# Performance work log

Hardware: AMD Instinct MI355X
Metric: run time of the kernel (lower is better)

## Reference

```python
import jax, jax.numpy as jnp
import numpy as np

B, T, E, H = 2, 2048, 1024, 16
D = E // H            # head dim = 64
ROT = D // 2          # rotary_dim = 32 (only first half of head dim is rotated)
THETA = 10000.0


def _rope(x):
    # x: (B, H, T, D). Faithful to rotary_embedding_torch.rotate_queries_or_keys
    # with dim=ROT: rotate first ROT features, interleaved-pair style, pass rest.
    t = x.shape[-2]
    inv = 1.0 / (THETA ** (jnp.arange(0, ROT, 2, dtype=jnp.float32) / ROT))   # (ROT//2,)
    freqs = jnp.arange(t, dtype=jnp.float32)[:, None] * inv[None, :]          # (T, ROT//2)
    freqs = jnp.repeat(freqs, 2, axis=-1)                                      # (T, ROT)
    cos, sin = jnp.cos(freqs), jnp.sin(freqs)
    xr, xp = x[..., :ROT], x[..., ROT:]
    p = xr.reshape(*xr.shape[:-1], ROT // 2, 2)
    rot = jnp.stack((-p[..., 1], p[..., 0]), axis=-1).reshape(xr.shape)
    return jnp.concatenate([xr * cos + rot * sin, xp], axis=-1)


def setup_inputs() -> dict:
    key = jax.random.key(0)
    k1, k2, k3 = jax.random.split(key, 3)
    query = jax.random.normal(k1, (B, T, E), dtype=jnp.float32)
    inputs = {
        "query": query,
        "key": query,            # ignored (cross_attention=False)
        "value": query,          # ignored
        "padding_mask": jnp.ones((B, T), dtype=bool),
        "in_proj_weight": jax.random.uniform(k2, (3 * E, E), dtype=jnp.float32),
        "out_proj_weight": jax.random.normal(k3, (E, E), dtype=jnp.float32) * (E ** -0.5),
    }
    return inputs


def reference(query, key, value, padding_mask, in_proj_weight, out_proj_weight):
    # cross_attention=False: key/value are overwritten by query
    key = query
    value = query
    q = query @ in_proj_weight[:E].T
    k = key @ in_proj_weight[E:2 * E].T
    v = value @ in_proj_weight[2 * E:].T
    # NOTE: raw reshape (B,T,E)->(B,H,T,D), exactly as in the torch module
    q = q.reshape(B, H, T, D)
    k = k.reshape(B, H, T, D)
    v = v.reshape(B, H, T, D)
    q = _rope(q)
    k = _rope(k)   # causal self-attention path: rotate keys too
    causal = jnp.tril(jnp.ones((T, T), dtype=bool))                 # (T, T)
    mask = causal[None, None] & padding_mask[:, None, None, :]      # (B,1,T,T) -> broadcast over H
    scores = jnp.einsum("bhqd,bhkd->bhqk", q, k) / jnp.sqrt(jnp.float32(D))
    scores = jnp.where(mask, scores, -jnp.inf)
    attn = jax.nn.softmax(scores, axis=-1)
    x = jnp.einsum("bhqk,bhkd->bhqd", attn, v)
    x = x.reshape(B, T, E)      # raw reshape back, as in torch
    return x @ out_proj_weight.T
```

## Files before the change

### kernel.cpp

```cpp
#include <hip/hip_runtime.h>
#include <stdint.h>

#define T_ 2048
#define E_ 1024

typedef __attribute__((ext_vector_type(8))) __bf16 bf16x8;
typedef __attribute__((ext_vector_type(4))) float f32x4;

__device__ __forceinline__ void gload_lds16(const void* g, void* l) {
  __builtin_amdgcn_global_load_lds(
      (const __attribute__((address_space(1))) unsigned int*)g,
      (__attribute__((address_space(3))) unsigned int*)l, 16, 0, 0);
}

__global__ __launch_bounds__(256) void k_prep(const float4* __restrict__ q,
                                              ushort4* __restrict__ xh,
                                              ushort4* __restrict__ xl,
                                              const float4* __restrict__ win,
                                              ushort4* __restrict__ whh,
                                              ushort4* __restrict__ whl,
                                              const float4* __restrict__ wout,
                                              ushort4* __restrict__ wob,
                                              float2* __restrict__ cs) {
  const int b = blockIdx.x, tid = threadIdx.x;
  if (b < 7168) {
    const float4* src;
    ushort4 *hi, *lo;
    int i;
    if (b < 4096) { src = q; hi = xh; lo = xl; i = b * 256 + tid; }
    else          { src = win; hi = whh; lo = whl; i = (b - 4096) * 256 + tid; }
    float4 x = src[i];
    float xs[4] = {x.x, x.y, x.z, x.w};
    union { __bf16 bb[4]; ushort4 u; } H, L;
#pragma unroll
    for (int jj = 0; jj < 4; ++jj) {
      __bf16 h = (__bf16)xs[jj];
      H.bb[jj] = h;
      L.bb[jj] = (__bf16)(xs[jj] - (float)h);
    }
    hi[i] = H.u;
    lo[i] = L.u;
  } else if (b < 8192) {
    int i = (b - 7168) * 256 + tid;
    float4 x = wout[i];
    float xs[4] = {x.x, x.y, x.z, x.w};
    union { __bf16 bb[4]; ushort4 u; } H;
#pragma unroll
    for (int jj = 0; jj < 4; ++jj) H.bb[jj] = (__bf16)xs[jj];
    wob[i] = H.u;
  } else {
    int i = (b - 8192) * 256 + tid;
    int t = i >> 4, f = i & 15;
    double inv = pow(10000.0, -(double)f / 16.0);
    double ang = (double)t * inv;
    cs[i] = make_float2((float)cos(ang), (float)sin(ang));
  }
}

__global__ __launch_bounds__(256) void k_proj(const __bf16* __restrict__ xh,
                                              const __bf16* __restrict__ xl,
                                              const __bf16* __restrict__ whh,
                                              const __bf16* __restrict__ whl,
                                              const float2* __restrict__ cs,
                                              __bf16* __restrict__ qhi,
                                              __bf16* __restrict__ qlo,
                                              __bf16* __restrict__ khi,
                                              __bf16* __restrict__ klo,
                                              __bf16* __restrict__ v16t) {
  __shared__ __align__(16) __bf16 AsH[128 * 64];
  __shared__ __align__(16) __bf16 BsH[128 * 64];
  __shared__ __align__(16) __bf16 AsL[128 * 64];
  __shared__ __align__(16) __bf16 BsL[128 * 64];
  const int tid = threadIdx.x, lane = tid & 63, w = tid >> 6;
  const int g = lane >> 4, d = lane & 15;
  const int lr8 = lane >> 3;
  const int swz8 = ((lane & 7) ^ lr8) * 8;
  const int rsl = d & 7;
  const int K = 1024;

  if (blockIdx.x < 512) {
    const int bi = blockIdx.x;
    const int bx = (bi >> 3) & 15;
    const int by = ((bi & 7) << 2) | ((bi >> 7) & 3);
    const int wm = w >> 1, wn = w & 1;
    const int m0 = by * 128, n0 = bx * 128;

    f32x4 acc[4][4];
#pragma unroll
    for (int i = 0; i < 4; ++i)
#pragma unroll
      for (int j = 0; j < 4; ++j) acc[i][j] = (f32x4)(0.0f);

    for (int k0 = 0; k0 < K; k0 += 64) {
      __syncthreads();
#pragma unroll
      for (int c = 0; c < 4; ++c) {
        const int rr = c * 32 + w * 8 + lr8;
        const int ldo = (c * 32 + w * 8) * 64;
        gload_lds16(xh + (size_t)(m0 + rr) * K + k0 + swz8, &AsH[ldo]);
        gload_lds16(xl + (size_t)(m0 + rr) * K + k0 + swz8, &AsL[ldo]);
        gload_lds16(whh + (size_t)(n0 + rr) * K + k0 + swz8, &BsH[ldo]);
        gload_lds16(whl + (size_t)(n0 + rr) * K + k0 + swz8, &BsL[ldo]);
      }
      __syncthreads();
#pragma unroll
      for (int k2 = 0; k2 < 2; ++k2) {
        const int sl = ((k2 * 4 + g) ^ rsl) * 8;
        bf16x8 bh[4], bl[4];
#pragma unroll
        for (int j = 0; j < 4; ++j) {
          const int r = wn * 64 + j * 16 + d;
          bh[j] = *(const bf16x8*)&BsH[r * 64 + sl];
          bl[j] = *(const bf16x8*)&BsL[r * 64 + sl];
        }
#pragma unroll
        for (int i = 0; i < 4; ++i) {
          const int r = wm * 64 + i * 16 + d;
          const bf16x8 ahf = *(const bf16x8*)&AsH[r * 64 + sl];
          const bf16x8 alf = *(const bf16x8*)&AsL[r * 64 + sl];
#pragma unroll
          for (int j = 0; j < 4; ++j) {
            acc[i][j] = __builtin_amdgcn_mfma_f32_16x16x32_bf16(ahf, bh[j], acc[i][j], 0, 0, 0);
            acc[i][j] = __builtin_amdgcn_mfma_f32_16x16x32_bf16(alf, bh[j], acc[i][j], 0, 0, 0);
            acc[i][j] = __builtin_amdgcn_mfma_f32_16x16x32_bf16(ahf, bl[j], acc[i][j], 0, 0, 0);
          }
        }
      }
    }

#pragma unroll
    for (int i = 0; i < 4; ++i) {
      const int rbase = m0 + (w >> 1) * 64 + i * 16 + g * 4;
#pragma unroll
      for (int j = 0; j < 4; ++j) {
        const int col = n0 + (w & 1) * 64 + j * 16 + d;
#pragma unroll
        for (int r = 0; r < 4; ++r) {
          const float vv = acc[i][j][r];
          const int row = rbase + r;
          const float xp = __shfl_xor(vv, 1);
          const int which = col >> 10;
          const int cl = col & 1023;
          const int d2 = cl & 63;
          const int t2 = (row & 127) * 16 + (cl >> 6);
          float y;
          if (d2 < 32) {
            const float2 cse = cs[t2 * 16 + (d2 >> 1)];
            y = (d2 & 1) ? (vv * cse.x + xp * cse.y) : (vv * cse.x - xp * cse.y);
          } else {
            y = vv;
          }
          if (which == 0) y *= 0.18033688011112042f;
          const __bf16 hi = (__bf16)y;
          const __bf16 lo = (__bf16)(y - (float)hi);
          const size_t off = (size_t)row * 1024 + cl;
          (which ? khi : qhi)[off] = hi;
          (which ? klo : qlo)[off] = lo;
        }
      }
    }
  } else {
    const int bi = blockIdx.x - 512;
    const int bx = (bi >> 3) & 7;
    const int by = ((bi & 7) << 3) | ((bi >> 6) & 7);
    const int m0 = by * 64, n0 = bx * 128;
    const __bf16* Bv = whh + (size_t)2048 * 1024;

    f32x4 acc[4][2];
#pragma unroll
    for (int i = 0; i < 4; ++i)
#pragma unroll
      for (int j = 0; j < 2; ++j) acc[i][j] = (f32x4)(0.0f);

    for (int k0 = 0; k0 < K; k0 += 64) {
      __syncthreads();
#pragma unroll
      for (int c = 0; c < 2; ++c) {
        const int rr = c * 32 + w * 8 + lr8;
        gload_lds16(xh + (size_t)(m0 + rr) * K + k0 + swz8, &AsH[(c * 32 + w * 8) * 64]);
      }
#pragma unroll
      for (int c = 0; c < 4; ++c) {
        const int rr = c * 32 + w * 8 + lr8;
        gload_lds16(Bv + (size_t)(n0 + rr) * K + k0 + swz8, &BsH[(c * 32 + w * 8) * 64]);
      }
      __syncthreads();
#pragma unroll
      for (int k2 = 0; k2 < 2; ++k2) {
        const int sl = ((k2 * 4 + g) ^ rsl) * 8;
        bf16x8 bh[2], ah[4];
#pragma unroll
        for (int j = 0; j < 2; ++j)
          bh[j] = *(const bf16x8*)&BsH[(w * 32 + j * 16 + d) * 64 + sl];
#pragma unroll
        for (int i = 0; i < 4; ++i)
          ah[i] = *(const bf16x8*)&AsH[(i * 16 + d) * 64 + sl];
#pragma unroll
        for (int i = 0; i < 4; ++i)
#pragma unroll
          for (int j = 0; j < 2; ++j)
            acc[i][j] = __builtin_amdgcn_mfma_f32_16x16x32_bf16(ah[i], bh[j], acc[i][j], 0, 0, 0);
      }
    }

#pragma unroll
    for (int i = 0; i < 4; ++i) {
      const int rbase = m0 + i * 16 + g * 4;
#pragma unroll
      for (int j = 0; j < 2; ++j) {
        const int col = n0 + w * 32 + j * 16 + d;
#pragma unroll
        for (int r = 0; r < 4; ++r) {
          const int row = rbase + r;
          const int p = row >> 7;
          const int tp = ((row & 127) << 4) | (col >> 6);
          const int dp = col & 63;
          v16t[((size_t)p * 64 + dp) * 2048 + tp] = (__bf16)acc[i][j][r];
        }
      }
    }
  }
}

__global__ __launch_bounds__(256) void k_gemmout(const __bf16* __restrict__ Ah,
                                                 const __bf16* __restrict__ Bh,
                                                 float* __restrict__ C32) {
  __shared__ __align__(16) __bf16 As[64 * 64];
  __shared__ __align__(16) __bf16 Bs[128 * 64];
  const int bi = blockIdx.x;
  const int bx = (bi >> 3) & 7;
  const int by = ((bi & 7) << 3) | ((bi >> 6) & 7);
  const int tid = threadIdx.x, lane = tid & 63, w = tid >> 6;
  const int g = lane >> 4, d = lane & 15;
  const int m0 = by * 64, n0 = bx * 128;
  const int K = 1024, N = 1024;

  f32x4 acc[4][2];
#pragma unroll
  for (int i = 0; i < 4; ++i)
#pragma unroll
    for (int j = 0; j < 2; ++j) acc[i][j] = (f32x4)(0.0f);

  const int lr8 = lane >> 3;
  const int swz8 = ((lane & 7) ^ lr8) * 8;
  const int rsl = d & 7;

  for (int k0 = 0; k0 < K; k0 += 64) {
    __syncthreads();
#pragma unroll
    for (int c = 0; c < 2; ++c) {
      const int rr = c * 32 + w * 8 + lr8;
      gload_lds16(Ah + (size_t)(m0 + rr) * K + k0 + swz8, &As[(c * 32 + w * 8) * 64]);
    }
#pragma unroll
    for (int c = 0; c < 4; ++c) {
      const int rr = c * 32 + w * 8 + lr8;
      gload_lds16(Bh + (size_t)(n0 + rr) * K + k0 + swz8, &Bs[(c * 32 + w * 8) * 64]);
    }
    __syncthreads();
#pragma unroll
    for (int k2 = 0; k2 < 2; ++k2) {
      const int sl = ((k2 * 4 + g) ^ rsl) * 8;
      bf16x8 bh[2], ah[4];
#pragma unroll
      for (int j = 0; j < 2; ++j)
        bh[j] = *(const bf16x8*)&Bs[(w * 32 + j * 16 + d) * 64 + sl];
#pragma unroll
      for (int i = 0; i < 4; ++i)
        ah[i] = *(const bf16x8*)&As[(i * 16 + d) * 64 + sl];
#pragma unroll
      for (int i = 0; i < 4; ++i)
#pragma unroll
        for (int j = 0; j < 2; ++j)
          acc[i][j] = __builtin_amdgcn_mfma_f32_16x16x32_bf16(ah[i], bh[j], acc[i][j], 0, 0, 0);
    }
  }

#pragma unroll
  for (int i = 0; i < 4; ++i) {
    const int rbase = m0 + i * 16 + g * 4;
#pragma unroll
    for (int j = 0; j < 2; ++j) {
      const int col = n0 + w * 32 + j * 16 + d;
#pragma unroll
      for (int r = 0; r < 4; ++r)
        C32[(size_t)(rbase + r) * N + col] = acc[i][j][r];
    }
  }
}

__global__ __launch_bounds__(512, 4) void k_attn(const __bf16* __restrict__ qhi,
                                                 const __bf16* __restrict__ qlo,
                                                 const __bf16* __restrict__ khi,
                                                 const __bf16* __restrict__ klo,
                                                 const __bf16* __restrict__ v16t,
                                                 __bf16* __restrict__ x16,
                                                 float* __restrict__ po,
                                                 float* __restrict__ pm,
                                                 float* __restrict__ pl_) {
  __shared__ __align__(16) __bf16 KH[2][64 * 64];
  __shared__ __align__(16) __bf16 KL[2][64 * 64];
  __shared__ __align__(16) __bf16 VT[2][64 * 64];
  __shared__ __align__(16) __bf16 PL[8][16 * 72];

  const int bi = blockIdx.x;
  const int b = (bi >> 3) & 15;
  const int panel = (bi & 7) | (((bi >> 7) & 3) << 3);
  const int u0 = 9 * b;
  int qtA = 0;
  while (2 * (qtA + 1) * (qtA + 2) <= u0) ++qtA;
  const int cumA = 2 * qtA * (qtA + 1);
  const int cumB = 2 * (qtA + 1) * (qtA + 2);
  const int jloA = u0 - cumA;
  const bool two = (u0 + 9 > cumB);
  const int jhiA = two ? (cumB - 1 - cumA) : (u0 + 8 - cumA);
  const int jhiB = u0 + 8 - cumB;

  const int tid = threadIdx.x, lane = tid & 63, w = tid >> 6;
  const int g = lane >> 4, d = lane & 15;
  const size_t hb = (size_t)panel * T_ * 64;

  const int kr = tid >> 3, kc = tid & 7;
  const int swz = (kc ^ (kr & 7)) * 8;
  const __bf16* kB = khi + hb;
  const __bf16* lB = klo + hb;
  const __bf16* vB = v16t + (size_t)panel * (64 * T_);

#define STAGE(j, bb)                                                        \
  {                                                                         \
    gload_lds16(kB + (size_t)((j) * 64 + kr) * 64 + swz, &KH[bb][w * 512]); \
    gload_lds16(lB + (size_t)((j) * 64 + kr) * 64 + swz, &KL[bb][w * 512]); \
    gload_lds16(vB + (size_t)kr * T_ + (j) * 64 + swz, &VT[bb][w * 512]);   \
  }

  int cur = 0;
  STAGE(jloA, 0);

  for (int seg = 0; seg < 2; ++seg) {
    if (seg && !two) break;
    const int qt = qtA + seg;
    const int jlo = seg ? 0 : jloA;
    const int jhi = seg ? jhiB : jhiA;
    const int q0 = qt << 8;

    bf16x8 qh[2][2], ql[2][2];
#pragma unroll
    for (int rb = 0; rb < 2; ++rb) {
      const int rbi = w * 2 + rb;
      const size_t qrow = hb + (size_t)(q0 + rbi * 16 + d) * 64;
      qh[rb][0] = *(const bf16x8*)&qhi[qrow + g * 8];
      qh[rb][1] = *(const bf16x8*)&qhi[qrow + 32 + g * 8];
      ql[rb][0] = *(const bf16x8*)&qlo[qrow + g * 8];
      ql[rb][1] = *(const bf16x8*)&qlo[qrow + 32 + g * 8];
    }

    f32x4 o[2][4];
#pragma unroll
    for (int rb = 0; rb < 2; ++rb)
#pragma unroll
      for (int i = 0; i < 4; ++i) o[rb][i] = (f32x4)(0.0f);
    float m_[2] = {-__builtin_inff(), -__builtin_inff()};
    float l_[2] = {0.0f, 0.0f};

    for (int j = jlo; j <= jhi; ++j) {
      __syncthreads();
      if (j < jhi) {
        STAGE(j + 1, cur ^ 1);
      } else if (!seg && two) {
        STAGE(0, cur ^ 1);
      }

#pragma unroll
      for (int rb = 0; rb < 2; ++rb) {
        const int rbi = w * 2 + rb;
        const int qrow0 = q0 + rbi * 16;
        if (j * 64 > qrow0 + 15) continue;

        f32x4 s[4];
        __builtin_amdgcn_s_setprio(1);
#pragma unroll
        for (int f = 0; f < 4; ++f) {
          f32x4 accs = (f32x4)(0.0f);
          const int colr = f * 16 + d;
#pragma unroll
          for (int ds = 0; ds < 2; ++ds) {
            const int slot = ((ds * 4 + g) ^ (colr & 7)) * 8;
            const bf16x8 kf = *(const bf16x8*)&KH[cur][colr * 64 + slot];
            const bf16x8 lf = *(const bf16x8*)&KL[cur][colr * 64 + slot];
            accs = __builtin_amdgcn_mfma_f32_16x16x32_bf16(kf, qh[rb][ds], accs, 0, 0, 0);
            accs = __builtin_amdgcn_mfma_f32_16x16x32_bf16(kf, ql[rb][ds], accs, 0, 0, 0);
            accs = __builtin_amdgcn_mfma_f32_16x16x32_bf16(lf, qh[rb][ds], accs, 0, 0, 0);
          }
          s[f] = accs;
        }
        __builtin_amdgcn_s_setprio(0);

        if (j * 64 + 63 > qrow0) {
          const int qq = qrow0 + d;
#pragma unroll
          for (int f = 0; f < 4; ++f)
#pragma unroll
            for (int r = 0; r < 4; ++r) {
              const int kv = j * 64 + f * 16 + g * 4 + r;
              if (kv > qq) s[f][r] = -30000.0f;
            }
        }

        float pmax = fmaxf(fmaxf(s[0][0], s[0][1]), fmaxf(s[0][2], s[0][3]));
#pragma unroll
        for (int f = 1; f < 4; ++f)
          pmax = fmaxf(pmax, fmaxf(fmaxf(s[f][0], s[f][1]), fmaxf(s[f][2], s[f][3])));
        pmax = fmaxf(pmax, __shfl_xor(pmax, 16));
        pmax = fmaxf(pmax, __shfl_xor(pmax, 32));

        if (!__all(pmax - m_[rb] <= 11.5f)) {
          const float mnew = fmaxf(m_[rb], pmax);
          const float fac = exp2f(m_[rb] - mnew);
          m_[rb] = mnew;
          float facr[4];
#pragma unroll
          for (int r = 0; r < 4; ++r)
            facr[r] = __shfl(fac, (lane & 48) | (g * 4 + r));
#pragma unroll
          for (int ni = 0; ni < 4; ++ni)
#pragma unroll
            for (int r = 0; r < 4; ++r) o[rb][ni][r] *= facr[r];
          l_[rb] *= fac;
        }

        float sum = 0.0f;
#pragma unroll
        for (int f = 0; f < 4; ++f) {
          union { __bf16 bb[4]; ushort4 u4; } pk;
#pragma unroll
          for (int r = 0; r < 4; ++r) {
            const float pv = exp2f(s[f][r] - m_[rb]);
            sum += pv;
            pk.bb[r] = (__bf16)pv;
          }
          *(ushort4*)&PL[w][d * 72 + f * 16 + g * 4] = pk.u4;
        }
        sum += __shfl_xor(sum, 16);
        sum += __shfl_xor(sum, 32);
        l_[rb] += sum;

        __builtin_amdgcn_s_setprio(1);
#pragma unroll
        for (int ks = 0; ks < 2; ++ks) {
          const bf16x8 pa = *(const bf16x8*)&PL[w][d * 72 + ks * 32 + g * 8];
#pragma unroll
          for (int ni = 0; ni < 4; ++ni) {
            const bf16x8 vf =
                *(const bf16x8*)&VT[cur][(ni * 16 + d) * 64 + (((ks * 4 + g) ^ (d & 7)) * 8)];
            o[rb][ni] = __builtin_amdgcn_mfma_f32_16x16x32_bf16(pa, vf, o[rb][ni], 0, 0, 0);
          }
        }
        __builtin_amdgcn_s_setprio(0);
      }
      cur ^= 1;
    }

    if (jlo == 0 && jhi == 4 * qt + 3) {
#pragma unroll
      for (int rb = 0; rb < 2; ++rb) {
        const int rbi = w * 2 + rb;
        float lr[4];
#pragma unroll
        for (int r = 0; r < 4; ++r)
          lr[r] = __shfl(l_[rb], (lane & 48) | (g * 4 + r));
#pragma unroll
        for (int ni = 0; ni < 4; ++ni)
#pragma unroll
          for (int r = 0; r < 4; ++r) {
            const size_t row = hb + (size_t)(q0 + rbi * 16 + g * 4 + r) * 64;
            x16[row + ni * 16 + d] = (__bf16)(o[rb][ni][r] / lr[r]);
          }
      }
    } else {
      const int slot = panel * 23 + b + qt;
#pragma unroll
      for (int rb = 0; rb < 2; ++rb) {
        const int rbi = w * 2 + rb;
#pragma unroll
        for (int ni = 0; ni < 4; ++ni)
#pragma unroll
          for (int r = 0; r < 4; ++r) {
            const int rowin = rbi * 16 + g * 4 + r;
            po[(size_t)slot * 16384 + rowin * 64 + ni * 16 + d] = o[rb][ni][r];
          }
        if (g == 0) {
          pm[slot * 256 + rbi * 16 + d] = m_[rb];
          pl_[slot * 256 + rbi * 16 + d] = l_[rb];
        }
      }
    }
  }
#undef STAGE
}

__global__ __launch_bounds__(256) void k_combine(const float* __restrict__ po,
                                                 const float* __restrict__ pm,
                                                 const float* __restrict__ pl_,
                                                 __bf16* __restrict__ x16) {
  const int bi = blockIdx.x;
  const int p = (bi & 7) | ((bi / 3584) << 3);
  const int li = ((bi >> 3) % 448) * 256 + threadIdx.x;
  const int d = li & 63;
  const int t2 = 256 + (li >> 6);
  const int qt = t2 >> 8;
  const int rowin = t2 & 255;
  const int cq = 2 * qt * (qt + 1);
  const int nc = (cq + 4 * qt + 3) / 9 - cq / 9 + 1;
  const int s0 = p * 23 + cq / 9 + qt;
  float M = -__builtin_inff();
  for (int s = 0; s < nc; ++s) M = fmaxf(M, pm[(s0 + s) * 256 + rowin]);
  float L = 0.0f, O = 0.0f;
  for (int s = 0; s < nc; ++s) {
    const float ww = exp2f(pm[(s0 + s) * 256 + rowin] - M);
    L += pl_[(s0 + s) * 256 + rowin] * ww;
    O += po[(size_t)(s0 + s) * 16384 + rowin * 64 + d] * ww;
  }
  x16[((size_t)p * T_ + t2) * 64 + d] = (__bf16)(O / L);
}

extern "C" void kernel_launch(void* const* d_in, const int* in_sizes, int n_in,
                              void* d_out, int out_size, void* d_ws, size_t ws_size,
                              hipStream_t stream) {
  const float* query = (const float*)d_in[0];
  const float* win = (const float*)d_in[4];
  const float* wout = (const float*)d_in[5];
  float* out = (float*)d_out;

  const size_t MB = 1024 * 1024;
  const size_t KB = 1024;
  char* ws = (char*)d_ws;
  __bf16* xh = (__bf16*)(ws);
  __bf16* xl = (__bf16*)(ws + 8 * MB);
  __bf16* whh = (__bf16*)(ws + 16 * MB);
  __bf16* whl = (__bf16*)(ws + 22 * MB);
  float* po = (float*)(ws);
  __bf16* v16t = (__bf16*)(ws + 46 * MB);
  __bf16* qhi = (__bf16*)(ws + 54 * MB);
  __bf16* qlo = (__bf16*)(ws + 62 * MB);
  __bf16* khi = (__bf16*)(ws + 70 * MB);
  __bf16* klo = (__bf16*)(ws + 78 * MB);
  __bf16* wob = (__bf16*)(ws + 86 * MB);
  float* pm = (float*)(ws + 88 * MB);
  float* pl_ = (float*)(ws + 88 * MB + 768 * KB);
  float2* cs = (float2*)(ws + 89 * MB + 512 * KB);
  __bf16* x16 = (__bf16*)(ws + 54 * MB);

  k_prep<<<8320, 256, 0, stream>>>((const float4*)query, (ushort4*)xh, (ushort4*)xl,
                                   (const float4*)win, (ushort4*)whh, (ushort4*)whl,
                                   (const float4*)wout, (ushort4*)wob, cs);

  k_proj<<<1024, 256, 0, stream>>>(xh, xl, whh, whl, cs, qhi, qlo, khi, klo, v16t);

  k_attn<<<512, 512, 0, stream>>>(qhi, qlo, khi, klo, v16t, x16, po, pm, pl_);

  k_combine<<<14336, 256, 0, stream>>>(po, pm, pl_, x16);

  k_gemmout<<<512, 256, 0, stream>>>(x16, wob, out);
}
```

Measured before the change: 186.7 us.

## Use 512-thread blocks in projection GEMM and enlarge V tile to 128x128

The projection kernel now launches 512 threads (8 waves) per block. Each wave computes a 64x32 sub-tile instead of 64x64, which cuts accumulator registers and raises waves per CU. The V-projection path moves from 64x128 to 128x128 tiles, so the total grid shrinks from 1024 to 768 blocks and the V path reuses more data per load. The trade-off is fewer blocks, and each wave re-reads A fragments from LDS with less reuse of the B fragments.

```diff
diff --git a/kernel.cpp b/kernel.cpp
--- a/kernel.cpp
+++ b/kernel.cpp
@@ -57,16 +57,16 @@
   }
 }
 
-__global__ __launch_bounds__(256) void k_proj(const __bf16* __restrict__ xh,
-                                              const __bf16* __restrict__ xl,
-                                              const __bf16* __restrict__ whh,
-                                              const __bf16* __restrict__ whl,
-                                              const float2* __restrict__ cs,
-                                              __bf16* __restrict__ qhi,
-                                              __bf16* __restrict__ qlo,
-                                              __bf16* __restrict__ khi,
-                                              __bf16* __restrict__ klo,
-                                              __bf16* __restrict__ v16t) {
+__global__ __launch_bounds__(512, 4) void k_proj(const __bf16* __restrict__ xh,
+                                                 const __bf16* __restrict__ xl,
+                                                 const __bf16* __restrict__ whh,
+                                                 const __bf16* __restrict__ whl,
+                                                 const float2* __restrict__ cs,
+                                                 __bf16* __restrict__ qhi,
+                                                 __bf16* __restrict__ qlo,
+                                                 __bf16* __restrict__ khi,
+                                                 __bf16* __restrict__ klo,
+                                                 __bf16* __restrict__ v16t) {
   __shared__ __align__(16) __bf16 AsH[128 * 64];
   __shared__ __align__(16) __bf16 BsH[128 * 64];
   __shared__ __align__(16) __bf16 AsL[128 * 64];
@@ -76,27 +76,27 @@
   const int lr8 = lane >> 3;
   const int swz8 = ((lane & 7) ^ lr8) * 8;
   const int rsl = d & 7;
+  const int wm = w >> 2, wn = w & 3;
   const int K = 1024;
 
   if (blockIdx.x < 512) {
     const int bi = blockIdx.x;
     const int bx = (bi >> 3) & 15;
     const int by = ((bi & 7) << 2) | ((bi >> 7) & 3);
-    const int wm = w >> 1, wn = w & 1;
     const int m0 = by * 128, n0 = bx * 128;
 
-    f32x4 acc[4][4];
+    f32x4 acc[4][2];
 #pragma unroll
     for (int i = 0; i < 4; ++i)
 #pragma unroll
-      for (int j = 0; j < 4; ++j) acc[i][j] = (f32x4)(0.0f);
+      for (int j = 0; j < 2; ++j) acc[i][j] = (f32x4)(0.0f);
 
     for (int k0 = 0; k0 < K; k0 += 64) {
       __syncthreads();
 #pragma unroll
-      for (int c = 0; c < 4; ++c) {
-        const int rr = c * 32 + w * 8 + lr8;
-        const int ldo = (c * 32 + w * 8) * 64;
+      for (int c = 0; c < 2; ++c) {
+        const int rr = c * 64 + w * 8 + lr8;
+        const int ldo = (c * 64 + w * 8) * 64;
         gload_lds16(xh + (size_t)(m0 + rr) * K + k0 + swz8, &AsH[ldo]);
         gload_lds16(xl + (size_t)(m0 + rr) * K + k0 + swz8, &AsL[ldo]);
         gload_lds16(whh + (size_t)(n0 + rr) * K + k0 + swz8, &BsH[ldo]);
@@ -106,10 +106,10 @@
 #pragma unroll
       for (int k2 = 0; k2 < 2; ++k2) {
         const int sl = ((k2 * 4 + g) ^ rsl) * 8;
-        bf16x8 bh[4], bl[4];
-#pragma unroll
-        for (int j = 0; j < 4; ++j) {
-          const int r = wn * 64 + j * 16 + d;
+        bf16x8 bh[2], bl[2];
+#pragma unroll
+        for (int j = 0; j < 2; ++j) {
+          const int r = wn * 32 + j * 16 + d;
           bh[j] = *(const bf16x8*)&BsH[r * 64 + sl];
           bl[j] = *(const bf16x8*)&BsL[r * 64 + sl];
         }
@@ -119,7 +119,7 @@
           const bf16x8 ahf = *(const bf16x8*)&AsH[r * 64 + sl];
           const bf16x8 alf = *(const bf16x8*)&AsL[r * 64 + sl];
 #pragma unroll
-          for (int j = 0; j < 4; ++j) {
+          for (int j = 0; j < 2; ++j) {
             acc[i][j] = __builtin_amdgcn_mfma_f32_16x16x32_bf16(ahf, bh[j], acc[i][j], 0, 0, 0);
             acc[i][j] = __builtin_amdgcn_mfma_f32_16x16x32_bf16(alf, bh[j], acc[i][j], 0, 0, 0);
             acc[i][j] = __builtin_amdgcn_mfma_f32_16x16x32_bf16(ahf, bl[j], acc[i][j], 0, 0, 0);
@@ -130,10 +130,10 @@
 
 #pragma unroll
     for (int i = 0; i < 4; ++i) {
-      const int rbase = m0 + (w >> 1) * 64 + i * 16 + g * 4;
-#pragma unroll
-      for (int j = 0; j < 4; ++j) {
-        const int col = n0 + (w & 1) * 64 + j * 16 + d;
+      const int rbase = m0 + wm * 64 + i * 16 + g * 4;
+#pragma unroll
+      for (int j = 0; j < 2; ++j) {
+        const int col = n0 + wn * 32 + j * 16 + d;
 #pragma unroll
         for (int r = 0; r < 4; ++r) {
           const float vv = acc[i][j][r];
@@ -160,10 +160,10 @@
       }
     }
   } else {
-    const int bi = blockIdx.x - 512;
-    const int bx = (bi >> 3) & 7;
-    const int by = ((bi & 7) << 3) | ((bi >> 6) & 7);
-    const int m0 = by * 64, n0 = bx * 128;
+    const int bv = blockIdx.x - 512;
+    const int bx = (bv >> 3) & 7;
+    const int by = ((bv & 7) << 2) | ((bv >> 6) & 3);
+    const int m0 = by * 128, n0 = bx * 128;
     const __bf16* Bv = whh + (size_t)2048 * 1024;
 
     f32x4 acc[4][2];
@@ -176,39 +176,35 @@
       __syncthreads();
 #pragma unroll
       for (int c = 0; c < 2; ++c) {
-        const int rr = c * 32 + w * 8 + lr8;
-        gload_lds16(xh + (size_t)(m0 + rr) * K + k0 + swz8, &AsH[(c * 32 + w * 8) * 64]);
-      }
-#pragma unroll
-      for (int c = 0; c < 4; ++c) {
-        const int rr = c * 32 + w * 8 + lr8;
-        gload_lds16(Bv + (size_t)(n0 + rr) * K + k0 + swz8, &BsH[(c * 32 + w * 8) * 64]);
+        const int rr = c * 64 + w * 8 + lr8;
+        const int ldo = (c * 64 + w * 8) * 64;
+        gload_lds16(xh + (size_t)(m0 + rr) * K + k0 + swz8, &AsH[ldo]);
+        gload_lds16(Bv + (size_t)(n0 + rr) * K + k0 + swz8, &BsH[ldo]);
       }
       __syncthreads();
 #pragma unroll
       for (int k2 = 0; k2 < 2; ++k2) {
         const int sl = ((k2 * 4 + g) ^ rsl) * 8;
-        bf16x8 bh[2], ah[4];
+        bf16x8 bh[2];
 #pragma unroll
         for (int j = 0; j < 2; ++j)
-          bh[j] = *(const bf16x8*)&BsH[(w * 32 + j * 16 + d) * 64 + sl];
-#pragma unroll
-        for (int i = 0; i < 4; ++i)
-          ah[i] = *(const bf16x8*)&AsH[(i * 16 + d) * 64 + sl];
-#pragma unroll
-        for (int i = 0; i < 4; ++i)
+          bh[j] = *(const bf16x8*)&BsH[(wn * 32 + j * 16 + d) * 64 + sl];
+#pragma unroll
+        for (int i = 0; i < 4; ++i) {
+          const bf16x8 ah = *(const bf16x8*)&AsH[(wm * 64 + i * 16 + d) * 64 + sl];
 #pragma unroll
           for (int j = 0; j < 2; ++j)
-            acc[i][j] = __builtin_amdgcn_mfma_f32_16x16x32_bf16(ah[i], bh[j], acc[i][j], 0, 0, 0);
+            acc[i][j] = __builtin_amdgcn_mfma_f32_16x16x32_bf16(ah, bh[j], acc[i][j], 0, 0, 0);
+        }
       }
     }
 
 #pragma unroll
     for (int i = 0; i < 4; ++i) {
-      const int rbase = m0 + i * 16 + g * 4;
+      const int rbase = m0 + wm * 64 + i * 16 + g * 4;
 #pragma unroll
       for (int j = 0; j < 2; ++j) {
-        const int col = n0 + w * 32 + j * 16 + d;
+        const int col = n0 + wn * 32 + j * 16 + d;
 #pragma unroll
         for (int r = 0; r < 4; ++r) {
           const int row = rbase + r;
@@ -554,7 +550,7 @@
                                    (const float4*)win, (ushort4*)whh, (ushort4*)whl,
                                    (const float4*)wout, (ushort4*)wob, cs);
 
-  k_proj<<<1024, 256, 0, stream>>>(xh, xl, whh, whl, cs, qhi, qlo, khi, klo, v16t);
+  k_proj<<<768, 512, 0, stream>>>(xh, xl, whh, whl, cs, qhi, qlo, khi, klo, v16t);
 
   k_attn<<<512, 512, 0, stream>>>(qhi, qlo, khi, klo, v16t, x16, po, pm, pl_);
 
```

New measurement: 198.2 us. 1.06x slower.
